# Kernel tuning notes

Hardware: AMD Instinct MI355X
Metric: run time of the kernel (lower is better)

## Reference

```python
import jax, jax.numpy as jnp
import numpy as np

N_MLP = 1024  # number of independent tiny MLPs
D_IN, D_HID, D_OUT = 2, 4, 1
B = 16384


def setup_inputs() -> dict:
    key = jax.random.key(0)
    k = jax.random.split(key, 6)
    x = jax.random.normal(k[0], (B, N_MLP), dtype=jnp.float32)
    x_aug = jax.random.normal(k[1], (B, N_MLP), dtype=jnp.float32)
    # Stacked per-MLP parameters (nn.Linear default init ~ U(-1/sqrt(fan_in), 1/sqrt(fan_in)))
    s1 = 1.0 / np.sqrt(D_IN)
    s2 = 1.0 / np.sqrt(D_HID)
    W1 = jax.random.uniform(k[2], (N_MLP, D_HID, D_IN), jnp.float32, -s1, s1)
    b1 = jax.random.uniform(k[3], (N_MLP, D_HID), jnp.float32, -s1, s1)
    W2 = jax.random.uniform(k[4], (N_MLP, D_OUT, D_HID), jnp.float32, -s2, s2)
    b2 = jax.random.uniform(k[5], (N_MLP, D_OUT), jnp.float32, -s2, s2)
    return {"x": x, "x_aug": x_aug, "W1": W1, "b1": b1, "W2": W2, "b2": b2}


def reference(x, x_aug, W1, b1, W2, b2):
    # data: [B, N, 2] — pair (original, augmented) per feature
    data = jnp.stack([x, x_aug], axis=-1)
    # batched tiny GEMM across the N_MLP axis: [B,N,2] x [N,4,2] -> [B,N,4]
    h = jax.nn.relu(jnp.einsum('bne,nhe->bnh', data, W1) + b1)
    # [B,N,4] x [N,1,4] -> [B,N,1]
    o = jnp.einsum('bnh,noh->bno', h, W2) + b2
    # concat over dim1 of per-MLP [B,1] outputs == squeeze -> [B,N]; mean over N -> [B]
    return jnp.mean(o[..., 0], axis=1)
```

## Files before the change

kernel.cpp:

```cpp
#include <hip/hip_runtime.h>


constexpr int N_MLP = 1024;
constexpr int BATCH = 16384;
constexpr int ROWS = 8;
constexpr int NTHREADS = 256;
constexpr int NQ = N_MLP / NTHREADS;

__global__ __launch_bounds__(256)
void zero_out_kernel(float* __restrict__ out) {
    out[blockIdx.x * 256 + threadIdx.x] = 0.0f;
}

__global__ __launch_bounds__(NTHREADS, 6)
void disc_mlp_kernel(const float* __restrict__ x,
                     const float* __restrict__ xa,
                     const float* __restrict__ W1,
                     const float* __restrict__ b1,
                     const float* __restrict__ W2,
                     const float* __restrict__ b2,
                     float* __restrict__ out)
{
    const int t  = threadIdx.x;
    const int q  = blockIdx.x & (NQ - 1);
    const int rb = blockIdx.x >> 2;
    const int b0 = rb * ROWS;
    const int n  = q * NTHREADS + t;

    const float4 p0 = reinterpret_cast<const float4*>(W1)[(size_t)n * 2];
    const float4 p1 = reinterpret_cast<const float4*>(W1)[(size_t)n * 2 + 1];
    const float4 bb = reinterpret_cast<const float4*>(b1)[n];
    const float4 ww = reinterpret_cast<const float4*>(W2)[n];
    const float  b2r = b2[n];

    const size_t base = (size_t)b0 * N_MLP + n;

    const float x0 = x[base + 0 * N_MLP];
    const float x1 = x[base + 1 * N_MLP];
    const float x2 = x[base + 2 * N_MLP];
    const float x3 = x[base + 3 * N_MLP];
    const float x4 = x[base + 4 * N_MLP];
    const float x5 = x[base + 5 * N_MLP];
    const float x6 = x[base + 6 * N_MLP];
    const float x7 = x[base + 7 * N_MLP];
    const float a0 = xa[base + 0 * N_MLP];
    const float a1 = xa[base + 1 * N_MLP];
    const float a2 = xa[base + 2 * N_MLP];
    const float a3 = xa[base + 3 * N_MLP];
    const float a4 = xa[base + 4 * N_MLP];
    const float a5 = xa[base + 5 * N_MLP];
    const float a6 = xa[base + 6 * N_MLP];
    const float a7 = xa[base + 7 * N_MLP];

    const float A[4]  = {p0.x, p0.z, p1.x, p1.z};
    const float C[4]  = {p0.y, p0.w, p1.y, p1.w};
    const float B1r[4] = {bb.x, bb.y, bb.z, bb.w};
    const float V[4]  = {ww.x, ww.y, ww.z, ww.w};

    const float xe[ROWS]  = {x0, x1, x2, x3, x4, x5, x6, x7};
    const float xae[ROWS] = {a0, a1, a2, a3, a4, a5, a6, a7};

    float acc[ROWS];
#pragma unroll
    for (int r = 0; r < ROWS; ++r) {
        float s = b2r;
#pragma unroll
        for (int j = 0; j < 4; ++j) {
            float h = fmaf(A[j], xe[r], fmaf(C[j], xae[r], B1r[j]));
            h = fmaxf(h, 0.0f);
            s = fmaf(V[j], h, s);
        }
        acc[r] = s;
    }

    __shared__ float lds[NTHREADS / 64][ROWS];
    const int lane = t & 63;
    const int wave = t >> 6;
#pragma unroll
    for (int r = 0; r < ROWS; ++r) {
        float v = acc[r];
        v += __shfl_down(v, 32);
        v += __shfl_down(v, 16);
        v += __shfl_down(v, 8);
        v += __shfl_down(v, 4);
        v += __shfl_down(v, 2);
        v += __shfl_down(v, 1);
        if (lane == 0) lds[wave][r] = v;
    }
    __syncthreads();
    if (t < ROWS) {
        float s = (lds[0][t] + lds[1][t]) + (lds[2][t] + lds[3][t]);
        atomicAdd(out + b0 + t, s * (1.0f / (float)N_MLP));
    }
}

extern "C" void kernel_launch(void* const* d_in, const int* in_sizes, int n_in,
                              void* d_out, int out_size, void* d_ws, size_t ws_size,
                              hipStream_t stream) {
    const float* x  = (const float*)d_in[0];
    const float* xa = (const float*)d_in[1];
    const float* W1 = (const float*)d_in[2];
    const float* b1 = (const float*)d_in[3];
    const float* W2 = (const float*)d_in[4];
    const float* b2 = (const float*)d_in[5];
    float* out = (float*)d_out;

    zero_out_kernel<<<BATCH / 256, 256, 0, stream>>>(out);
    disc_mlp_kernel<<<(BATCH / ROWS) * NQ, NTHREADS, 0, stream>>>(x, xa, W1, b1, W2, b2, out);
}
```

Measured before the change: 150.9 us.

## Stage input rows into LDS via direct global-to-LDS loads and double rows per block

Replaces per-thread scalar global loads of x and x_aug with 16-byte-wide global_load_lds transfers into shared memory buffers, then reads them back from LDS. The rows per block go from 8 to 16, which halves the block count, the weight reloads and the atomics. The aim is wider memory transactions with fewer instructions and less per-row overhead. In exchange the kernel uses more LDS and adds a barrier, and the launch bounds occupancy hint is removed.

```diff
diff --git a/kernel.cpp b/kernel.cpp
--- a/kernel.cpp
+++ b/kernel.cpp
@@ -3,16 +3,20 @@
 
 constexpr int N_MLP = 1024;
 constexpr int BATCH = 16384;
-constexpr int ROWS = 8;
+constexpr int ROWS = 16;
 constexpr int NTHREADS = 256;
-constexpr int NQ = N_MLP / NTHREADS;
+constexpr int QN = 256;
+constexpr int NQ = N_MLP / QN;
+
+typedef __attribute__((address_space(3))) void lds_void;
+typedef const __attribute__((address_space(1))) void gbl_void;
 
 __global__ __launch_bounds__(256)
 void zero_out_kernel(float* __restrict__ out) {
     out[blockIdx.x * 256 + threadIdx.x] = 0.0f;
 }
 
-__global__ __launch_bounds__(NTHREADS, 6)
+__global__ __launch_bounds__(NTHREADS)
 void disc_mlp_kernel(const float* __restrict__ x,
                      const float* __restrict__ xa,
                      const float* __restrict__ W1,
@@ -21,11 +25,17 @@
                      const float* __restrict__ b2,
                      float* __restrict__ out)
 {
-    const int t  = threadIdx.x;
+    __shared__ float xbuf[ROWS * QN];
+    __shared__ float abuf[ROWS * QN];
+    __shared__ float red[NTHREADS / 64][ROWS];
+
+    const int t    = threadIdx.x;
+    const int lane = t & 63;
+    const int wave = t >> 6;
     const int q  = blockIdx.x & (NQ - 1);
     const int rb = blockIdx.x >> 2;
     const int b0 = rb * ROWS;
-    const int n  = q * NTHREADS + t;
+    const int n  = q * QN + t;
 
     const float4 p0 = reinterpret_cast<const float4*>(W1)[(size_t)n * 2];
     const float4 p1 = reinterpret_cast<const float4*>(W1)[(size_t)n * 2 + 1];
@@ -33,49 +43,42 @@
     const float4 ww = reinterpret_cast<const float4*>(W2)[n];
     const float  b2r = b2[n];
 
-    const size_t base = (size_t)b0 * N_MLP + n;
+    const float* gx = x  + (size_t)b0 * N_MLP + q * QN;
+    const float* ga = xa + (size_t)b0 * N_MLP + q * QN;
+#pragma unroll
+    for (int i = 0; i < ROWS / 4; ++i) {
+        const int r = wave * (ROWS / 4) + i;
+        const float* srcx = gx + (size_t)r * N_MLP + lane * 4;
+        const float* srca = ga + (size_t)r * N_MLP + lane * 4;
+        __builtin_amdgcn_global_load_lds((gbl_void*)srcx,
+                                         (lds_void*)&xbuf[r * QN + lane * 4],
+                                         16, 0, 0);
+        __builtin_amdgcn_global_load_lds((gbl_void*)srca,
+                                         (lds_void*)&abuf[r * QN + lane * 4],
+                                         16, 0, 0);
+    }
+    __syncthreads();
 
-    const float x0 = x[base + 0 * N_MLP];
-    const float x1 = x[base + 1 * N_MLP];
-    const float x2 = x[base + 2 * N_MLP];
-    const float x3 = x[base + 3 * N_MLP];
-    const float x4 = x[base + 4 * N_MLP];
-    const float x5 = x[base + 5 * N_MLP];
-    const float x6 = x[base + 6 * N_MLP];
-    const float x7 = x[base + 7 * N_MLP];
-    const float a0 = xa[base + 0 * N_MLP];
-    const float a1 = xa[base + 1 * N_MLP];
-    const float a2 = xa[base + 2 * N_MLP];
-    const float a3 = xa[base + 3 * N_MLP];
-    const float a4 = xa[base + 4 * N_MLP];
-    const float a5 = xa[base + 5 * N_MLP];
-    const float a6 = xa[base + 6 * N_MLP];
-    const float a7 = xa[base + 7 * N_MLP];
-
-    const float A[4]  = {p0.x, p0.z, p1.x, p1.z};
-    const float C[4]  = {p0.y, p0.w, p1.y, p1.w};
+    const float A[4]   = {p0.x, p0.z, p1.x, p1.z};
+    const float C[4]   = {p0.y, p0.w, p1.y, p1.w};
     const float B1r[4] = {bb.x, bb.y, bb.z, bb.w};
-    const float V[4]  = {ww.x, ww.y, ww.z, ww.w};
-
-    const float xe[ROWS]  = {x0, x1, x2, x3, x4, x5, x6, x7};
-    const float xae[ROWS] = {a0, a1, a2, a3, a4, a5, a6, a7};
+    const float V[4]   = {ww.x, ww.y, ww.z, ww.w};
 
     float acc[ROWS];
 #pragma unroll
     for (int r = 0; r < ROWS; ++r) {
+        const float xe  = xbuf[r * QN + t];
+        const float xae = abuf[r * QN + t];
         float s = b2r;
 #pragma unroll
         for (int j = 0; j < 4; ++j) {
-            float h = fmaf(A[j], xe[r], fmaf(C[j], xae[r], B1r[j]));
+            float h = fmaf(A[j], xe, fmaf(C[j], xae, B1r[j]));
             h = fmaxf(h, 0.0f);
             s = fmaf(V[j], h, s);
         }
         acc[r] = s;
     }
 
-    __shared__ float lds[NTHREADS / 64][ROWS];
-    const int lane = t & 63;
-    const int wave = t >> 6;
 #pragma unroll
     for (int r = 0; r < ROWS; ++r) {
         float v = acc[r];
@@ -85,11 +88,11 @@
         v += __shfl_down(v, 4);
         v += __shfl_down(v, 2);
         v += __shfl_down(v, 1);
-        if (lane == 0) lds[wave][r] = v;
+        if (lane == 0) red[wave][r] = v;
     }
     __syncthreads();
     if (t < ROWS) {
-        float s = (lds[0][t] + lds[1][t]) + (lds[2][t] + lds[3][t]);
+        float s = (red[0][t] + red[1][t]) + (red[2][t] + red[3][t]);
         atomicAdd(out + b0 + t, s * (1.0f / (float)N_MLP));
     }
 }
```

Result: no change. 150.2 us (-0.4%).
